# Kernel optimization log

Hardware: AMD Instinct MI355X
Metric: run time of the kernel (lower is better)

## Reference

```python
import jax, jax.numpy as jnp
import numpy as np

N_NODES = 50000
N_EDGES = 800000
NODE_F = 128
EDGE_F = 64
OUT_F = 128


def setup_inputs() -> dict:
    key = jax.random.key(0)
    k1, k2, k3, k4, k5 = jax.random.split(key, 5)
    x = jax.random.normal(k1, (N_NODES, NODE_F), dtype=jnp.float32)
    edge_index = jax.random.randint(k2, (2, N_EDGES), 0, N_NODES, dtype=jnp.int64)
    edge_attr = jax.random.normal(k3, (N_EDGES, EDGE_F), dtype=jnp.float32)
    # Linear(node_features + edge_features, out_features) params (torch default init scale)
    fan_in = NODE_F + EDGE_F
    bound = 1.0 / np.sqrt(fan_in)
    W = jax.random.uniform(k4, (fan_in, OUT_F), minval=-bound, maxval=bound, dtype=jnp.float32)
    b = jax.random.uniform(k5, (OUT_F,), minval=-bound, maxval=bound, dtype=jnp.float32)
    return {"x": x, "edge_index": edge_index, "edge_attr": edge_attr, "W": W, "b": b}


def reference(x, edge_index, edge_attr, W, b):
    # PyG source_to_target flow: x_j = x[src], aggregate at dst
    src = edge_index[0]
    dst = edge_index[1]
    x_j = x[src]                                   # [E, node_f] gather
    feats = jnp.concatenate([edge_attr, x_j], axis=1)  # [E, edge_f + node_f]
    msg = jax.nn.relu(feats @ W + b)               # [E, out_f] Linear + ReLU
    out = jax.ops.segment_sum(msg, dst, num_segments=x.shape[0])  # scatter-add
    return out
```

## Files before the change

kernel.cpp:

```cpp
#include <hip/hip_runtime.h>
#include <hip/hip_bf16.h>

#define N_NODES 50000
#define N_EDGES 800000
#define NODE_F  128
#define EDGE_F  64
#define OUT_F   128

#define NCH ((N_NODES + 255) / 256)
#define EPW 128
#define NRANGES (N_EDGES / EPW)

typedef __attribute__((ext_vector_type(8))) short short8;
typedef __attribute__((ext_vector_type(4))) short short4v;
typedef __attribute__((ext_vector_type(4))) float floatx4;

__device__ __forceinline__ unsigned short f2bf(float f) {
    unsigned int u = __float_as_uint(f);
    u += 0x7fffu + ((u >> 16) & 1u);
    return (unsigned short)(u >> 16);
}

__device__ __forceinline__ short8 cvt8(floatx4 v0, floatx4 v1) {
    union { __hip_bfloat162 h[4]; short8 s; } u;
    u.h[0] = __float22bfloat162_rn(make_float2(v0[0], v0[1]));
    u.h[1] = __float22bfloat162_rn(make_float2(v0[2], v0[3]));
    u.h[2] = __float22bfloat162_rn(make_float2(v1[0], v1[1]));
    u.h[3] = __float22bfloat162_rn(make_float2(v1[2], v1[3]));
    return u.s;
}

#define TILE_N1 32
#define N_NTILES ((N_NODES + TILE_N1 - 1) / TILE_N1)
#define LDS_STRIDE1 136

__global__ __launch_bounds__(256, 4) void node_kernel(
    const float* __restrict__ x,
    const float* __restrict__ W,
    const float* __restrict__ bias,
    float*       __restrict__ Y)
{
    __shared__ __align__(16) unsigned short xs[TILE_N1][LDS_STRIDE1];

    const int tid  = threadIdx.x;
    const int wave = tid >> 6;
    const int lane = tid & 63;
    const int col  = lane & 15;
    const int quad = lane >> 4;
    const int wbase = wave * 32;

    const float* __restrict__ Wx = W + EDGE_F * OUT_F;

    short8 bfr[4][2];
    #pragma unroll
    for (int kc = 0; kc < 4; ++kc) {
        #pragma unroll
        for (int ns = 0; ns < 2; ++ns) {
            const int n = wbase + ns * 16 + col;
            const int krow = kc * 32 + quad * 8;
            short8 v;
            #pragma unroll
            for (int j = 0; j < 8; ++j)
                v[j] = (short)f2bf(Wx[(krow + j) * OUT_F + n]);
            bfr[kc][ns] = v;
        }
    }
    const float b0 = bias[wbase + col];
    const float b1 = bias[wbase + 16 + col];

    for (int tile = blockIdx.x; tile < N_NTILES; tile += gridDim.x) {
        const int n0 = tile * TILE_N1;
        {
            const int e   = tid >> 3;
            const int sub = tid & 7;
            const int node = n0 + e;
            const float* __restrict__ xr = x + (size_t)node * NODE_F;
            #pragma unroll
            for (int i = 0; i < 4; ++i) {
                const int fi = sub + 8 * i;
                floatx4 v = {0.f, 0.f, 0.f, 0.f};
                if (node < N_NODES) v = *(const floatx4*)(xr + fi * 4);
                union { __hip_bfloat162 h[2]; short4v s; } u;
                u.h[0] = __float22bfloat162_rn(make_float2(v[0], v[1]));
                u.h[1] = __float22bfloat162_rn(make_float2(v[2], v[3]));
                *(short4v*)&xs[e][fi * 4] = u.s;
            }
        }
        __syncthreads();

        floatx4 acc[2][2] = {};
        #pragma unroll
        for (int kc = 0; kc < 4; ++kc) {
            short8 a0 = *(const short8*)&xs[col     ][kc * 32 + quad * 8];
            short8 a1 = *(const short8*)&xs[16 + col][kc * 32 + quad * 8];
            acc[0][0] = __builtin_amdgcn_mfma_f32_16x16x32_bf16(a0, bfr[kc][0], acc[0][0], 0, 0, 0);
            acc[0][1] = __builtin_amdgcn_mfma_f32_16x16x32_bf16(a0, bfr[kc][1], acc[0][1], 0, 0, 0);
            acc[1][0] = __builtin_amdgcn_mfma_f32_16x16x32_bf16(a1, bfr[kc][0], acc[1][0], 0, 0, 0);
            acc[1][1] = __builtin_amdgcn_mfma_f32_16x16x32_bf16(a1, bfr[kc][1], acc[1][1], 0, 0, 0);
        }

        #pragma unroll
        for (int ms = 0; ms < 2; ++ms) {
            #pragma unroll
            for (int r = 0; r < 4; ++r) {
                const int m = ms * 16 + quad * 4 + r;
                const int node = n0 + m;
                if (node < N_NODES) {
                    float* yrow = Y + (size_t)node * OUT_F + wbase;
                    yrow[col]      = acc[ms][0][r] + b0;
                    yrow[16 + col] = acc[ms][1][r] + b1;
                }
            }
        }
        __syncthreads();
    }
}

__global__ void hist_kernel(const int* __restrict__ edge_index, int* __restrict__ hist) {
    const int* dstp = edge_index + N_EDGES;
    for (int i = blockIdx.x * blockDim.x + threadIdx.x; i < N_EDGES;
         i += gridDim.x * blockDim.x)
        atomicAdd(&hist[dstp[i]], 1);
}

__global__ void scan1_kernel(const int* __restrict__ hist, int* __restrict__ chunkSum) {
    __shared__ int s[256];
    const int c = blockIdx.x, t = threadIdx.x, idx = c * 256 + t;
    s[t] = (idx < N_NODES) ? hist[idx] : 0;
    __syncthreads();
    for (int off = 128; off > 0; off >>= 1) {
        if (t < off) s[t] += s[t + off];
        __syncthreads();
    }
    if (t == 0) chunkSum[c] = s[0];
}

__global__ void scan2_kernel(const int* __restrict__ chunkSum, int* __restrict__ chunkBase) {
    __shared__ int s[256];
    const int t = threadIdx.x;
    s[t] = (t < NCH) ? chunkSum[t] : 0;
    __syncthreads();
    for (int off = 1; off < 256; off <<= 1) {
        int u = (t >= off) ? s[t - off] : 0;
        __syncthreads();
        s[t] += u;
        __syncthreads();
    }
    if (t < NCH) chunkBase[t] = (t == 0) ? 0 : s[t - 1];
}

__global__ void scan3_kernel(const int* __restrict__ hist, const int* __restrict__ chunkBase,
                             int* __restrict__ row_off, int* __restrict__ cursor) {
    __shared__ int s[256];
    const int c = blockIdx.x, t = threadIdx.x, idx = c * 256 + t;
    const int v = (idx < N_NODES) ? hist[idx] : 0;
    s[t] = v;
    __syncthreads();
    for (int off = 1; off < 256; off <<= 1) {
        int u = (t >= off) ? s[t - off] : 0;
        __syncthreads();
        s[t] += u;
        __syncthreads();
    }
    const int excl = s[t] - v + chunkBase[c];
    if (idx < N_NODES) { row_off[idx] = excl; cursor[idx] = excl; }
    if (c == 0 && t == 0) row_off[N_NODES] = N_EDGES;
}

__device__ __forceinline__ int lbound(const int* __restrict__ ro, int target) {
    int lo = 0, hi = N_NODES;
    while (lo < hi) {
        const int mid = (lo + hi) >> 1;
        if (ro[mid] < target) lo = mid + 1; else hi = mid;
    }
    return lo;
}

__global__ void range_kernel(const int* __restrict__ row_off, int* __restrict__ range_start) {
    const int rg = blockIdx.x * blockDim.x + threadIdx.x;
    if (rg <= NRANGES) range_start[rg] = row_off[lbound(row_off, rg * EPW)];
}

__global__ void scatter_kernel(const int* __restrict__ edge_index,
                               int* __restrict__ cursor, int2* __restrict__ sorted) {
    const int* srcp = edge_index;
    const int* dstp = edge_index + N_EDGES;
    for (int i = blockIdx.x * blockDim.x + threadIdx.x; i < N_EDGES;
         i += gridDim.x * blockDim.x) {
        const int d = dstp[i];
        const int p = atomicAdd(&cursor[d], 1);
        sorted[p] = make_int2(i, (int)(((unsigned)srcp[i] << 16) | (unsigned)d));
    }
}

__global__ __launch_bounds__(256, 6) void edge_gemm(
    const float* __restrict__ edge_attr,
    const float* __restrict__ W,
    const float* __restrict__ Y,
    const int*   __restrict__ range_start,
    const int2*  __restrict__ sorted,
    float*       __restrict__ out)
{
    __shared__ float CT[4][16][68];

    const int tid  = threadIdx.x;
    const int wave = tid >> 6;
    const int lane = tid & 63;
    const int col  = lane & 15;
    const int quad = lane >> 4;
    const int p    = wave & 1;

    short8 bfr[2][4];
    #pragma unroll
    for (int kc = 0; kc < 2; ++kc) {
        #pragma unroll
        for (int ns = 0; ns < 4; ++ns) {
            const int n = p * 64 + ns * 16 + col;
            const int krow = kc * 32 + quad * 8;
            short8 v;
            #pragma unroll
            for (int j = 0; j < 8; ++j)
                v[j] = (short)f2bf(W[(krow + j) * OUT_F + n]);
            bfr[kc][ns] = v;
        }
    }

    float* __restrict__ obase = out + p * 64 + lane;

    const int grange = blockIdx.x * 2 + (wave >> 1);
    const int stride = gridDim.x * 2;

    for (int rg = grange; rg < NRANGES; rg += stride) {
        const int eb = range_start[rg];
        const int ee = range_start[rg + 1];
        if (eb >= ee) continue;

        int   cur = -1;
        float s   = 0.f;

        int2 me = sorted[min(eb + col, ee - 1)];
        short8 a[2];
        {
            const float* __restrict__ ar = edge_attr + (size_t)me.x * EDGE_F;
            #pragma unroll
            for (int kc = 0; kc < 2; ++kc)
                a[kc] = cvt8(*(const floatx4*)(ar + kc * 32 + quad * 8),
                             *(const floatx4*)(ar + kc * 32 + quad * 8 + 4));
        }

        for (int t0 = eb; t0 < ee; t0 += 16) {
            floatx4 acc[4];
            #pragma unroll
            for (int r = 0; r < 4; ++r) {
                const int src = (int)((unsigned)__shfl(me.y, quad * 4 + r) >> 16);
                const float* __restrict__ yr = Y + (size_t)src * OUT_F + p * 64;
                #pragma unroll
                for (int ns = 0; ns < 4; ++ns)
                    acc[ns][r] = yr[ns * 16 + col];
            }

            #pragma unroll
            for (int kc = 0; kc < 2; ++kc) {
                #pragma unroll
                for (int ns = 0; ns < 4; ++ns)
                    acc[ns] = __builtin_amdgcn_mfma_f32_16x16x32_bf16(a[kc], bfr[kc][ns], acc[ns], 0, 0, 0);
            }

            #pragma unroll
            for (int r = 0; r < 4; ++r) {
                const bool rvalid = (t0 + quad * 4 + r) < ee;
                #pragma unroll
                for (int ns = 0; ns < 4; ++ns)
                    CT[wave][quad * 4 + r][ns * 16 + col] =
                        rvalid ? fmaxf(acc[ns][r], 0.f) : 0.f;
            }
            __builtin_amdgcn_wave_barrier();

            const int t1 = t0 + 16;
            int2 me2;
            if (t1 < ee) me2 = sorted[min(t1 + col, ee - 1)];

            float cv[16];
            #pragma unroll
            for (int m = 0; m < 16; ++m) cv[m] = CT[wave][m][lane];

            const int mez = me.y;
            #pragma unroll
            for (int m = 0; m < 16; ++m) {
                const int d = (int)((unsigned)__builtin_amdgcn_readlane(mez, m) & 0xffffu);
                if (d != cur) {
                    if (cur >= 0) obase[(size_t)cur * OUT_F] = s;
                    cur = d; s = 0.f;
                }
                s += cv[m];
            }
            cur = __builtin_amdgcn_readfirstlane(cur);
            __builtin_amdgcn_wave_barrier();

            if (t1 < ee) {
                me = me2;
                const float* __restrict__ ar = edge_attr + (size_t)me.x * EDGE_F;
                #pragma unroll
                for (int kc = 0; kc < 2; ++kc)
                    a[kc] = cvt8(*(const floatx4*)(ar + kc * 32 + quad * 8),
                                 *(const floatx4*)(ar + kc * 32 + quad * 8 + 4));
            }
        }
        if (cur >= 0) obase[(size_t)cur * OUT_F] = s;
    }
}

__global__ __launch_bounds__(256, 3) void edge_kernel_atomic(
    const float* __restrict__ edge_attr,
    const int*   __restrict__ edge_index,
    const float* __restrict__ W,
    const float* __restrict__ Y,
    float*       __restrict__ out)
{
    const int lane = threadIdx.x & 63;
    const int col  = lane & 15;
    const int quad = lane >> 4;

    short8 bfr[2][8];
    #pragma unroll
    for (int kc = 0; kc < 2; ++kc)
        #pragma unroll
        for (int ns = 0; ns < 8; ++ns) {
            const int n = ns * 16 + col;
            const int krow = kc * 32 + quad * 8;
            short8 v;
            #pragma unroll
            for (int j = 0; j < 8; ++j)
                v[j] = (short)f2bf(W[(krow + j) * OUT_F + n]);
            bfr[kc][ns] = v;
        }

    const int* __restrict__ srcp = edge_index;
    const int* __restrict__ dstp = edge_index + N_EDGES;

    const int gwave  = blockIdx.x * 4 + (threadIdx.x >> 6);
    const int nwaves = gridDim.x * 4;

    for (int t = gwave; t < N_EDGES / 16; t += nwaves) {
        const int e0 = t * 16;
        const float* __restrict__ ar = edge_attr + (size_t)(e0 + col) * EDGE_F;
        short8 a[2];
        #pragma unroll
        for (int kc = 0; kc < 2; ++kc)
            a[kc] = cvt8(*(const floatx4*)(ar + kc * 32 + quad * 8),
                         *(const floatx4*)(ar + kc * 32 + quad * 8 + 4));
        int sr[4], dr[4];
        #pragma unroll
        for (int r = 0; r < 4; ++r) {
            sr[r] = srcp[e0 + quad * 4 + r];
            dr[r] = dstp[e0 + quad * 4 + r];
        }
        floatx4 acc[8];
        #pragma unroll
        for (int ns = 0; ns < 8; ++ns)
            #pragma unroll
            for (int r = 0; r < 4; ++r)
                acc[ns][r] = Y[(size_t)sr[r] * OUT_F + ns * 16 + col];
        #pragma unroll
        for (int kc = 0; kc < 2; ++kc)
            #pragma unroll
            for (int ns = 0; ns < 8; ++ns)
                acc[ns] = __builtin_amdgcn_mfma_f32_16x16x32_bf16(a[kc], bfr[kc][ns], acc[ns], 0, 0, 0);
        #pragma unroll
        for (int ns = 0; ns < 8; ++ns)
            #pragma unroll
            for (int r = 0; r < 4; ++r) {
                const float v = acc[ns][r];
                if (v > 0.0f)
                    atomicAdd(out + (size_t)dr[r] * OUT_F + ns * 16 + col, v);
            }
    }
}

extern "C" void kernel_launch(void* const* d_in, const int* in_sizes, int n_in,
                              void* d_out, int out_size, void* d_ws, size_t ws_size,
                              hipStream_t stream) {
    const float* x          = (const float*)d_in[0];
    const int*   edge_index = (const int*)  d_in[1];
    const float* edge_attr  = (const float*)d_in[2];
    const float* W          = (const float*)d_in[3];
    const float* bias       = (const float*)d_in[4];
    float*       out        = (float*)d_out;

    float* Y          = (float*)d_ws;
    int2*  sorted     = (int2*)(Y + (size_t)N_NODES * OUT_F);
    int*   hist       = (int*)(sorted + N_EDGES);
    int*   chunkSum   = hist + N_NODES;
    int*   chunkBase  = chunkSum + 256;
    int*   row_off    = chunkBase + 256;
    int*   cursor     = row_off + N_NODES + 1;
    int*   range_start= cursor + N_NODES;
    const size_t needed = (size_t)((char*)(range_start + NRANGES + 1) - (char*)d_ws);

    hipMemsetAsync(out, 0, (size_t)out_size * sizeof(float), stream);
    node_kernel<<<dim3(512), dim3(256), 0, stream>>>(x, W, bias, Y);

    if (ws_size < needed) {
        edge_kernel_atomic<<<dim3(1024), dim3(256), 0, stream>>>(edge_attr, edge_index, W, Y, out);
        return;
    }

    hipMemsetAsync(hist, 0, (size_t)N_NODES * sizeof(int), stream);
    hist_kernel   <<<dim3(2048), dim3(256), 0, stream>>>(edge_index, hist);
    scan1_kernel  <<<dim3(NCH),  dim3(256), 0, stream>>>(hist, chunkSum);
    scan2_kernel  <<<dim3(1),    dim3(256), 0, stream>>>(chunkSum, chunkBase);
    scan3_kernel  <<<dim3(NCH),  dim3(256), 0, stream>>>(hist, chunkBase, row_off, cursor);
    range_kernel  <<<dim3((NRANGES + 256) / 256), dim3(256), 0, stream>>>(row_off, range_start);
    scatter_kernel<<<dim3(2048), dim3(256), 0, stream>>>(edge_index, cursor, sorted);
    edge_gemm     <<<dim3(1536), dim3(256), 0, stream>>>(
        edge_attr, W, Y, range_start, sorted, out);
}
```

Measured before the change: 483.1 us.

## Fuse preprocessing kernels, zero only empty rows, and software-pipeline edge GEMM loads

Merges the node GEMM with the histogram, folds scan2 into scan3 (each block reduces the preceding chunk sums itself), and merges the range search with the scatter pass. The full output memset is replaced by zeroing only nodes with no incoming edges inside the scan kernel. The edge GEMM now launches one wave-pair per range and prefetches the next sorted indices and edge attributes one tile ahead, so memory latency overlaps compute. Fewer launches and less memset traffic are the intended savings. The costs are redundant chunk-sum reductions and extra register pressure from the prefetch.

```diff
diff --git a/kernel.cpp b/kernel.cpp
--- a/kernel.cpp
+++ b/kernel.cpp
@@ -33,14 +33,27 @@
 #define TILE_N1 32
 #define N_NTILES ((N_NODES + TILE_N1 - 1) / TILE_N1)
 #define LDS_STRIDE1 136
-
-__global__ __launch_bounds__(256, 4) void node_kernel(
+#define NODE_BLOCKS 782
+#define HIST_BLOCKS 1024
+
+__global__ __launch_bounds__(256, 4) void node_hist_kernel(
     const float* __restrict__ x,
     const float* __restrict__ W,
     const float* __restrict__ bias,
-    float*       __restrict__ Y)
+    float*       __restrict__ Y,
+    const int*   __restrict__ edge_index,
+    int*         __restrict__ hist)
 {
     __shared__ __align__(16) unsigned short xs[TILE_N1][LDS_STRIDE1];
+
+    if (blockIdx.x >= NODE_BLOCKS) {
+        const int* __restrict__ dstp = edge_index + N_EDGES;
+        const int stride = (gridDim.x - NODE_BLOCKS) * 256;
+        for (int i = (blockIdx.x - NODE_BLOCKS) * 256 + threadIdx.x; i < N_EDGES;
+             i += stride)
+            atomicAdd(&hist[dstp[i]], 1);
+        return;
+    }
 
     const int tid  = threadIdx.x;
     const int wave = tid >> 6;
@@ -68,7 +81,7 @@
     const float b0 = bias[wbase + col];
     const float b1 = bias[wbase + 16 + col];
 
-    for (int tile = blockIdx.x; tile < N_NTILES; tile += gridDim.x) {
+    for (int tile = blockIdx.x; tile < N_NTILES; tile += NODE_BLOCKS) {
         const int n0 = tile * TILE_N1;
         {
             const int e   = tid >> 3;
@@ -116,13 +129,6 @@
     }
 }
 
-__global__ void hist_kernel(const int* __restrict__ edge_index, int* __restrict__ hist) {
-    const int* dstp = edge_index + N_EDGES;
-    for (int i = blockIdx.x * blockDim.x + threadIdx.x; i < N_EDGES;
-         i += gridDim.x * blockDim.x)
-        atomicAdd(&hist[dstp[i]], 1);
-}
-
 __global__ void scan1_kernel(const int* __restrict__ hist, int* __restrict__ chunkSum) {
     __shared__ int s[256];
     const int c = blockIdx.x, t = threadIdx.x, idx = c * 256 + t;
@@ -135,24 +141,22 @@
     if (t == 0) chunkSum[c] = s[0];
 }
 
-__global__ void scan2_kernel(const int* __restrict__ chunkSum, int* __restrict__ chunkBase) {
+__global__ void scan23_kernel(const int* __restrict__ hist, const int* __restrict__ chunkSum,
+                              int* __restrict__ row_off, int* __restrict__ cursor,
+                              float* __restrict__ out) {
     __shared__ int s[256];
-    const int t = threadIdx.x;
-    s[t] = (t < NCH) ? chunkSum[t] : 0;
+    __shared__ int basev;
+    const int c = blockIdx.x, t = threadIdx.x, idx = c * 256 + t;
+
+    s[t] = (t < c) ? chunkSum[t] : 0;
     __syncthreads();
-    for (int off = 1; off < 256; off <<= 1) {
-        int u = (t >= off) ? s[t - off] : 0;
-        __syncthreads();
-        s[t] += u;
-        __syncthreads();
-    }
-    if (t < NCH) chunkBase[t] = (t == 0) ? 0 : s[t - 1];
-}
-
-__global__ void scan3_kernel(const int* __restrict__ hist, const int* __restrict__ chunkBase,
-                             int* __restrict__ row_off, int* __restrict__ cursor) {
-    __shared__ int s[256];
-    const int c = blockIdx.x, t = threadIdx.x, idx = c * 256 + t;
+    for (int off = 128; off > 0; off >>= 1) {
+        if (t < off) s[t] += s[t + off];
+        __syncthreads();
+    }
+    if (t == 0) basev = s[0];
+    __syncthreads();
+
     const int v = (idx < N_NODES) ? hist[idx] : 0;
     s[t] = v;
     __syncthreads();
@@ -162,8 +166,17 @@
         s[t] += u;
         __syncthreads();
     }
-    const int excl = s[t] - v + chunkBase[c];
-    if (idx < N_NODES) { row_off[idx] = excl; cursor[idx] = excl; }
+    const int excl = s[t] - v + basev;
+    if (idx < N_NODES) {
+        row_off[idx] = excl;
+        cursor[idx]  = excl;
+        if (v == 0) {
+            floatx4 z = {0.f, 0.f, 0.f, 0.f};
+            float* o = out + (size_t)idx * OUT_F;
+            #pragma unroll
+            for (int i = 0; i < 32; ++i) *(floatx4*)(o + i * 4) = z;
+        }
+    }
     if (c == 0 && t == 0) row_off[N_NODES] = N_EDGES;
 }
 
@@ -176,17 +189,23 @@
     return lo;
 }
 
-__global__ void range_kernel(const int* __restrict__ row_off, int* __restrict__ range_start) {
-    const int rg = blockIdx.x * blockDim.x + threadIdx.x;
-    if (rg <= NRANGES) range_start[rg] = row_off[lbound(row_off, rg * EPW)];
-}
-
-__global__ void scatter_kernel(const int* __restrict__ edge_index,
-                               int* __restrict__ cursor, int2* __restrict__ sorted) {
-    const int* srcp = edge_index;
-    const int* dstp = edge_index + N_EDGES;
-    for (int i = blockIdx.x * blockDim.x + threadIdx.x; i < N_EDGES;
-         i += gridDim.x * blockDim.x) {
+#define RS_RANGE_BLOCKS 32
+#define RS_SCATTER_BLOCKS 2048
+__global__ void range_scatter_kernel(const int* __restrict__ row_off,
+                                     const int* __restrict__ edge_index,
+                                     int* __restrict__ cursor,
+                                     int* __restrict__ range_start,
+                                     int2* __restrict__ sorted) {
+    if (blockIdx.x < RS_RANGE_BLOCKS) {
+        const int rg = blockIdx.x * 256 + threadIdx.x;
+        if (rg <= NRANGES) range_start[rg] = row_off[lbound(row_off, rg * EPW)];
+        return;
+    }
+    const int* __restrict__ srcp = edge_index;
+    const int* __restrict__ dstp = edge_index + N_EDGES;
+    const int stride = (gridDim.x - RS_RANGE_BLOCKS) * 256;
+    for (int i = (blockIdx.x - RS_RANGE_BLOCKS) * 256 + threadIdx.x; i < N_EDGES;
+         i += stride) {
         const int d = dstp[i];
         const int p = atomicAdd(&cursor[d], 1);
         sorted[p] = make_int2(i, (int)(((unsigned)srcp[i] << 16) | (unsigned)d));
@@ -227,29 +246,91 @@
 
     float* __restrict__ obase = out + p * 64 + lane;
 
-    const int grange = blockIdx.x * 2 + (wave >> 1);
-    const int stride = gridDim.x * 2;
-
-    for (int rg = grange; rg < NRANGES; rg += stride) {
-        const int eb = range_start[rg];
-        const int ee = range_start[rg + 1];
-        if (eb >= ee) continue;
-
-        int   cur = -1;
-        float s   = 0.f;
-
-        int2 me = sorted[min(eb + col, ee - 1)];
-        short8 a[2];
-        {
-            const float* __restrict__ ar = edge_attr + (size_t)me.x * EDGE_F;
-            #pragma unroll
-            for (int kc = 0; kc < 2; ++kc)
-                a[kc] = cvt8(*(const floatx4*)(ar + kc * 32 + quad * 8),
-                             *(const floatx4*)(ar + kc * 32 + quad * 8 + 4));
-        }
-
-        for (int t0 = eb; t0 < ee; t0 += 16) {
-            floatx4 acc[4];
+    const int rg = blockIdx.x * 2 + (wave >> 1);
+    if (rg >= NRANGES) return;
+
+    const int eb = range_start[rg];
+    const int ee = range_start[rg + 1];
+    if (eb >= ee) return;
+
+    int   cur = -1;
+    float s   = 0.f;
+
+    int2 me  = sorted[min(eb + col, ee - 1)];
+    int2 meN = me;
+    if (eb + 16 < ee) meN = sorted[min(eb + 16 + col, ee - 1)];
+
+    short8 a[2];
+    {
+        const float* __restrict__ ar = edge_attr + (size_t)me.x * EDGE_F;
+        a[0] = cvt8(*(const floatx4*)(ar + quad * 8),
+                    *(const floatx4*)(ar + quad * 8 + 4));
+        a[1] = cvt8(*(const floatx4*)(ar + 32 + quad * 8),
+                    *(const floatx4*)(ar + 32 + quad * 8 + 4));
+    }
+    floatx4 acc[4];
+    #pragma unroll
+    for (int r = 0; r < 4; ++r) {
+        const int src = (int)((unsigned)__shfl(me.y, quad * 4 + r) >> 16);
+        const float* __restrict__ yr = Y + (size_t)src * OUT_F + p * 64;
+        #pragma unroll
+        for (int ns = 0; ns < 4; ++ns)
+            acc[ns][r] = yr[ns * 16 + col];
+    }
+
+    for (int t0 = eb; t0 < ee; t0 += 16) {
+        const int t1 = t0 + 16;
+
+        #pragma unroll
+        for (int kc = 0; kc < 2; ++kc) {
+            #pragma unroll
+            for (int ns = 0; ns < 4; ++ns)
+                acc[ns] = __builtin_amdgcn_mfma_f32_16x16x32_bf16(a[kc], bfr[kc][ns], acc[ns], 0, 0, 0);
+        }
+
+        #pragma unroll
+        for (int r = 0; r < 4; ++r) {
+            const bool rvalid = (t0 + quad * 4 + r) < ee;
+            #pragma unroll
+            for (int ns = 0; ns < 4; ++ns)
+                CT[wave][quad * 4 + r][ns * 16 + col] =
+                    rvalid ? fmaxf(acc[ns][r], 0.f) : 0.f;
+        }
+        __builtin_amdgcn_wave_barrier();
+
+        int2 meNN = meN;
+        if (t1 + 16 < ee) meNN = sorted[min(t1 + 16 + col, ee - 1)];
+
+        floatx4 ra0, ra1, ra2, ra3;
+        if (t1 < ee) {
+            const float* __restrict__ arN = edge_attr + (size_t)meN.x * EDGE_F;
+            ra0 = *(const floatx4*)(arN + quad * 8);
+            ra1 = *(const floatx4*)(arN + quad * 8 + 4);
+            ra2 = *(const floatx4*)(arN + 32 + quad * 8);
+            ra3 = *(const floatx4*)(arN + 32 + quad * 8 + 4);
+        }
+
+        float cv[16];
+        #pragma unroll
+        for (int m = 0; m < 16; ++m) cv[m] = CT[wave][m][lane];
+
+        const int mez = me.y;
+        #pragma unroll
+        for (int m = 0; m < 16; ++m) {
+            const int d = (int)((unsigned)__builtin_amdgcn_readlane(mez, m) & 0xffffu);
+            if (d != cur) {
+                if (cur >= 0) obase[(size_t)cur * OUT_F] = s;
+                cur = d; s = 0.f;
+            }
+            s += cv[m];
+        }
+        cur = __builtin_amdgcn_readfirstlane(cur);
+        __builtin_amdgcn_wave_barrier();
+
+        me = meN; meN = meNN;
+        if (t1 < ee) {
+            a[0] = cvt8(ra0, ra1);
+            a[1] = cvt8(ra2, ra3);
             #pragma unroll
             for (int r = 0; r < 4; ++r) {
                 const int src = (int)((unsigned)__shfl(me.y, quad * 4 + r) >> 16);
@@ -258,56 +339,9 @@
                 for (int ns = 0; ns < 4; ++ns)
                     acc[ns][r] = yr[ns * 16 + col];
             }
-
-            #pragma unroll
-            for (int kc = 0; kc < 2; ++kc) {
-                #pragma unroll
-                for (int ns = 0; ns < 4; ++ns)
-                    acc[ns] = __builtin_amdgcn_mfma_f32_16x16x32_bf16(a[kc], bfr[kc][ns], acc[ns], 0, 0, 0);
-            }
-
-            #pragma unroll
-            for (int r = 0; r < 4; ++r) {
-                const bool rvalid = (t0 + quad * 4 + r) < ee;
-                #pragma unroll
-                for (int ns = 0; ns < 4; ++ns)
-                    CT[wave][quad * 4 + r][ns * 16 + col] =
-                        rvalid ? fmaxf(acc[ns][r], 0.f) : 0.f;
-            }
-            __builtin_amdgcn_wave_barrier();
-
-            const int t1 = t0 + 16;
-            int2 me2;
-            if (t1 < ee) me2 = sorted[min(t1 + col, ee - 1)];
-
-            float cv[16];
-            #pragma unroll
-            for (int m = 0; m < 16; ++m) cv[m] = CT[wave][m][lane];
-
-            const int mez = me.y;
-            #pragma unroll
-            for (int m = 0; m < 16; ++m) {
-                const int d = (int)((unsigned)__builtin_amdgcn_readlane(mez, m) & 0xffffu);
-                if (d != cur) {
-                    if (cur >= 0) obase[(size_t)cur * OUT_F] = s;
-                    cur = d; s = 0.f;
-                }
-                s += cv[m];
-            }
-            cur = __builtin_amdgcn_readfirstlane(cur);
-            __builtin_amdgcn_wave_barrier();
-
-            if (t1 < ee) {
-                me = me2;
-                const float* __restrict__ ar = edge_attr + (size_t)me.x * EDGE_F;
-                #pragma unroll
-                for (int kc = 0; kc < 2; ++kc)
-                    a[kc] = cvt8(*(const floatx4*)(ar + kc * 32 + quad * 8),
-                                 *(const floatx4*)(ar + kc * 32 + quad * 8 + 4));
-            }
-        }
-        if (cur >= 0) obase[(size_t)cur * OUT_F] = s;
-    }
+        }
+    }
+    if (cur >= 0) obase[(size_t)cur * OUT_F] = s;
 }
 
 __global__ __launch_bounds__(256, 3) void edge_kernel_atomic(
@@ -397,21 +431,21 @@
     int*   range_start= cursor + N_NODES;
     const size_t needed = (size_t)((char*)(range_start + NRANGES + 1) - (char*)d_ws);
 
-    hipMemsetAsync(out, 0, (size_t)out_size * sizeof(float), stream);
-    node_kernel<<<dim3(512), dim3(256), 0, stream>>>(x, W, bias, Y);
-
     if (ws_size < needed) {
+        hipMemsetAsync(out, 0, (size_t)out_size * sizeof(float), stream);
+        node_hist_kernel<<<dim3(NODE_BLOCKS), dim3(256), 0, stream>>>(
+            x, W, bias, Y, edge_index, (int*)nullptr);
         edge_kernel_atomic<<<dim3(1024), dim3(256), 0, stream>>>(edge_attr, edge_index, W, Y, out);
         return;
     }
 
     hipMemsetAsync(hist, 0, (size_t)N_NODES * sizeof(int), stream);
-    hist_kernel   <<<dim3(2048), dim3(256), 0, stream>>>(edge_index, hist);
-    scan1_kernel  <<<dim3(NCH),  dim3(256), 0, stream>>>(hist, chunkSum);
-    scan2_kernel  <<<dim3(1),    dim3(256), 0, stream>>>(chunkSum, chunkBase);
-    scan3_kernel  <<<dim3(NCH),  dim3(256), 0, stream>>>(hist, chunkBase, row_off, cursor);
-    range_kernel  <<<dim3((NRANGES + 256) / 256), dim3(256), 0, stream>>>(row_off, range_start);
-    scatter_kernel<<<dim3(2048), dim3(256), 0, stream>>>(edge_index, cursor, sorted);
-    edge_gemm     <<<dim3(1536), dim3(256), 0, stream>>>(
+    node_hist_kernel<<<dim3(NODE_BLOCKS + HIST_BLOCKS), dim3(256), 0, stream>>>(
+        x, W, bias, Y, edge_index, hist);
+    scan1_kernel   <<<dim3(NCH), dim3(256), 0, stream>>>(hist, chunkSum);
+    scan23_kernel  <<<dim3(NCH), dim3(256), 0, stream>>>(hist, chunkSum, row_off, cursor, out);
+    range_scatter_kernel<<<dim3(RS_RANGE_BLOCKS + RS_SCATTER_BLOCKS), dim3(256), 0, stream>>>(
+        row_off, edge_index, cursor, range_start, sorted);
+    edge_gemm<<<dim3((NRANGES + 1) / 2), dim3(256), 0, stream>>>(
         edge_attr, W, Y, range_start, sorted, out);
 }
```

Result: slower. 609.7 us (+26.2%).
